# Kernel optimization log

Measured on AMD Instinct MI355X. Metric: run time of the kernel, lower is better.

## Reference

```python
import jax, jax.numpy as jnp
import numpy as np

N_DELTA, N_THETA, N_GAMMA = 2, 4, 8
N_OSC = N_DELTA + N_THETA + N_GAMMA  # 14
INPUT_DIM = 512
N_CLASSES = 2
COUPLING = 1.5
DT = 0.01
N_STEPS = 100


def _natural_freqs():
    # Natural frequencies (Hz) per EEG band: delta ~2Hz, theta ~6Hz, gamma ~40Hz
    return jnp.concatenate([
        jnp.full((N_DELTA,), 2.0, dtype=jnp.float32),
        jnp.full((N_THETA,), 6.0, dtype=jnp.float32),
        jnp.full((N_GAMMA,), 40.0, dtype=jnp.float32),
    ])


def setup_inputs() -> dict:
    key = jax.random.key(0)
    k_x, k_win, k_wc = jax.random.split(key, 3)
    x = jax.random.normal(k_x, (4096, 64, INPUT_DIM), dtype=jnp.float32)
    W_in = jax.random.normal(k_win, (INPUT_DIM, N_OSC), dtype=jnp.float32) / np.sqrt(INPUT_DIM)
    b_in = jnp.zeros((N_OSC,), dtype=jnp.float32)
    omega = _natural_freqs()
    Wc = jax.random.normal(k_wc, (N_OSC, N_CLASSES), dtype=jnp.float32) / np.sqrt(N_OSC)
    bc = jnp.zeros((N_CLASSES,), dtype=jnp.float32)
    return {"x": x, "W_in": W_in, "b_in": b_in, "omega": omega, "Wc": Wc, "bc": bc}


def reference(x, W_in, b_in, omega, Wc, bc):
    # Mean-pool over the object/token dimension: [B,S,D] -> [B,D]
    if x.ndim == 3:
        x = x.mean(axis=1)
    # Project input features to initial oscillator phases: [B,14]
    theta0 = x @ W_in + b_in
    two_pi = jnp.float32(2.0 * np.pi)
    k_over_n = jnp.float32(COUPLING / N_OSC)
    dt = jnp.float32(DT)

    def step(theta, _):
        s = jnp.sin(theta)
        c = jnp.cos(theta)
        # mean-field Kuramoto coupling: sum_j sin(th_j - th_i) = S*cos(th_i) - C*sin(th_i)
        S = s.sum(axis=-1, keepdims=True)
        C = c.sum(axis=-1, keepdims=True)
        dtheta = two_pi * omega + k_over_n * (S * c - C * s)
        return theta + dt * dtheta, None

    theta, _ = jax.lax.scan(step, theta0, None, length=N_STEPS)
    h = jnp.cos(theta)  # oscillator readout: [B,14]
    logits = h @ Wc + bc
    return jax.nn.log_softmax(logits, axis=-1)
```

## Files before the change

kernel.cpp:

```cpp
#include <hip/hip_runtime.h>
#include <math.h>

#define SEQ   64
#define DIM   512
#define NOSC  14
#define NSTEP 100

typedef float f4 __attribute__((ext_vector_type(4)));

__device__ __forceinline__ float dpp_sum16(float v) {
    v += __int_as_float(__builtin_amdgcn_update_dpp(0, __float_as_int(v), 0xB1,  0xF, 0xF, true));
    v += __int_as_float(__builtin_amdgcn_update_dpp(0, __float_as_int(v), 0x4E,  0xF, 0xF, true));
    v += __int_as_float(__builtin_amdgcn_update_dpp(0, __float_as_int(v), 0x141, 0xF, 0xF, true));
    v += __int_as_float(__builtin_amdgcn_update_dpp(0, __float_as_int(v), 0x140, 0xF, 0xF, true));
    return v;
}

__device__ __forceinline__ void fast_sincos(float theta, float* s, float* c) {
    const float inv2pi = 0.15915494309189535f;
    float r = theta * inv2pi;
    r = r - floorf(r);
    *s = __builtin_amdgcn_sinf(r);
    *c = __builtin_amdgcn_cosf(r);
}

__global__ __launch_bounds__(256)
void fused_kernel(const float* __restrict__ x,
                  const float* __restrict__ W_in,
                  const float* __restrict__ b_in,
                  const float* __restrict__ omega,
                  const float* __restrict__ Wc,
                  const float* __restrict__ bc,
                  float* __restrict__ out)
{
    const int b = blockIdx.x;
    const int t = threadIdx.x;
    const int f = t & 127;
    const int shalf = t >> 7;

    const f4* xv = reinterpret_cast<const f4*>(x + (size_t)b * (SEQ * DIM));

    f4 acc = (f4)(0.0f);
    const int s0 = shalf * 32;
#pragma unroll 8
    for (int s = s0; s < s0 + 32; ++s) {
        f4 v = __builtin_nontemporal_load(&xv[s * (DIM / 4) + f]);
        acc += v;
    }

    __shared__ float meanv[DIM];
    __shared__ f4    part[128];
    __shared__ float pp[NOSC][16];

    if (shalf == 1) part[f] = acc;
    __syncthreads();
    if (shalf == 0) {
        f4 o = part[f];
        const float inv = 1.0f / (float)SEQ;
        meanv[4 * f + 0] = (acc[0] + o[0]) * inv;
        meanv[4 * f + 1] = (acc[1] + o[1]) * inv;
        meanv[4 * f + 2] = (acc[2] + o[2]) * inv;
        meanv[4 * f + 3] = (acc[3] + o[3]) * inv;
    }
    __syncthreads();

    if (t < NOSC * 16) {
        const int o  = t >> 4;
        const int ch = t & 15;
        float p = 0.f;
#pragma unroll 8
        for (int d = ch * 32; d < ch * 32 + 32; ++d)
            p += meanv[d] * W_in[d * NOSC + o];
        pp[o][ch] = p;
    }
    __syncthreads();

    if (t >= 16) return;

    const int  o    = t;
    const bool act  = (o < NOSC);
    const float mask = act ? 1.0f : 0.0f;
    const int   oc   = act ? o : (NOSC - 1);

    float theta = 0.0f;
    if (act) {
        theta = b_in[o];
#pragma unroll
        for (int ch = 0; ch < 16; ++ch) theta += pp[o][ch];
    }

    const float drift = 6.283185307179586f * omega[oc];
    const float kn = 1.5f / (float)NOSC;
    const float dt = 0.01f;

    for (int it = 0; it < NSTEP; ++it) {
        float s_, c_;
        fast_sincos(theta, &s_, &c_);
        s_ *= mask;
        c_ *= mask;
        const float S = dpp_sum16(s_);
        const float C = dpp_sum16(c_);
        theta += dt * (drift + kn * (S * c_ - C * s_));
    }

    float hs, hc;
    fast_sincos(theta, &hs, &hc);
    const float h = hc * mask;
    float z0 = dpp_sum16(h * Wc[oc * 2 + 0]);
    float z1 = dpp_sum16(h * Wc[oc * 2 + 1]);

    if (o == 0) {
        z0 += bc[0];
        z1 += bc[1];
        const float mx  = fmaxf(z0, z1);
        const float lse = mx + logf(expf(z0 - mx) + expf(z1 - mx));
        out[(size_t)b * 2 + 0] = z0 - lse;
        out[(size_t)b * 2 + 1] = z1 - lse;
    }
}

extern "C" void kernel_launch(void* const* d_in, const int* in_sizes, int n_in,
                              void* d_out, int out_size, void* d_ws, size_t ws_size,
                              hipStream_t stream)
{
    const float* x     = (const float*)d_in[0];
    const float* W_in  = (const float*)d_in[1];
    const float* b_in  = (const float*)d_in[2];
    const float* omega = (const float*)d_in[3];
    const float* Wc    = (const float*)d_in[4];
    const float* bc    = (const float*)d_in[5];
    float* out = (float*)d_out;

    const int B = in_sizes[0] / (SEQ * DIM);

    fused_kernel<<<B, 256, 0, stream>>>(x, W_in, b_in, omega, Wc, bc, out);
}
```

Baseline: 107.2 us.

## Process two rows per block, overlapping next-row loads with ODE integration

Each block now handles two batch rows. While a wavefront (threads 192+) runs the 100-step Kuramoto integration for the current row, threads 0-127 stream and mean-pool the next row into a double-buffered shared array. The aim is to hide the serial sincos/DPP loop behind memory traffic. In exchange, each row's pooling now uses only 128 threads with 64 serial loads instead of 256, the grid is halved, and the pipeline depth is only two, so latency hiding per block is limited.

```diff
diff --git a/kernel.cpp b/kernel.cpp
--- a/kernel.cpp
+++ b/kernel.cpp
@@ -5,6 +5,7 @@
 #define DIM   512
 #define NOSC  14
 #define NSTEP 100
+#define RPB   2
 
 typedef float f4 __attribute__((ext_vector_type(4)));
 
@@ -24,98 +25,112 @@
     *c = __builtin_amdgcn_cosf(r);
 }
 
-__global__ __launch_bounds__(256)
+__global__ __launch_bounds__(256, 8)
 void fused_kernel(const float* __restrict__ x,
                   const float* __restrict__ W_in,
                   const float* __restrict__ b_in,
                   const float* __restrict__ omega,
                   const float* __restrict__ Wc,
                   const float* __restrict__ bc,
-                  float* __restrict__ out)
+                  float* __restrict__ out, int B)
 {
-    const int b = blockIdx.x;
-    const int t = threadIdx.x;
-    const int f = t & 127;
-    const int shalf = t >> 7;
+    const int t    = threadIdx.x;
+    const int row0 = blockIdx.x * RPB;
 
-    const f4* xv = reinterpret_cast<const f4*>(x + (size_t)b * (SEQ * DIM));
-
-    f4 acc = (f4)(0.0f);
-    const int s0 = shalf * 32;
-#pragma unroll 8
-    for (int s = s0; s < s0 + 32; ++s) {
-        f4 v = __builtin_nontemporal_load(&xv[s * (DIM / 4) + f]);
-        acc += v;
-    }
-
-    __shared__ float meanv[DIM];
-    __shared__ f4    part[128];
+    __shared__ f4    mv[2][DIM / 4];
     __shared__ float pp[NOSC][16];
 
-    if (shalf == 1) part[f] = acc;
+    if (t < 128 && row0 < B) {
+        const f4* xv = reinterpret_cast<const f4*>(x + (size_t)row0 * (SEQ * DIM));
+        f4 acc = (f4)(0.0f);
+#pragma unroll 4
+        for (int s = 0; s < SEQ; ++s)
+            acc += __builtin_nontemporal_load(&xv[s * (DIM / 4) + t]);
+        mv[0][t] = acc * (1.0f / SEQ);
+    }
     __syncthreads();
-    if (shalf == 0) {
-        f4 o = part[f];
-        const float inv = 1.0f / (float)SEQ;
-        meanv[4 * f + 0] = (acc[0] + o[0]) * inv;
-        meanv[4 * f + 1] = (acc[1] + o[1]) * inv;
-        meanv[4 * f + 2] = (acc[2] + o[2]) * inv;
-        meanv[4 * f + 3] = (acc[3] + o[3]) * inv;
+    {
+        const float* m = reinterpret_cast<const float*>(mv[0]);
+        if (t < NOSC * 16) {
+            const int o  = t >> 4;
+            const int ch = t & 15;
+            float p = 0.f;
+#pragma unroll 8
+            for (int i = 0; i < 32; ++i) {
+                const int d = i * 16 + ch;
+                p += m[d] * W_in[d * NOSC + o];
+            }
+            pp[o][ch] = p;
+        }
     }
     __syncthreads();
 
-    if (t < NOSC * 16) {
-        const int o  = t >> 4;
-        const int ch = t & 15;
-        float p = 0.f;
+    for (int r = 0; r < RPB; ++r) {
+        const int nb = (r & 1) ^ 1;
+        if (t >= 192) {
+            const int lane = t - 192;
+            const int row  = row0 + r;
+            if (lane < 16 && row < B) {
+                const bool  act  = (lane < NOSC);
+                const float mask = act ? 1.0f : 0.0f;
+                const int   oc   = act ? lane : (NOSC - 1);
+
+                float theta = 0.0f;
+                if (act) {
+                    theta = b_in[lane];
+#pragma unroll
+                    for (int ch = 0; ch < 16; ++ch) theta += pp[lane][ch];
+                }
+                const float drift = 6.283185307179586f * omega[oc];
+                const float kn = 1.5f / (float)NOSC;
+                const float dt = 0.01f;
+
+                for (int it = 0; it < NSTEP; ++it) {
+                    float s_, c_;
+                    fast_sincos(theta, &s_, &c_);
+                    s_ *= mask; c_ *= mask;
+                    const float S = dpp_sum16(s_);
+                    const float C = dpp_sum16(c_);
+                    theta += dt * (drift + kn * (S * c_ - C * s_));
+                }
+
+                float hs, hc;
+                fast_sincos(theta, &hs, &hc);
+                const float h = hc * mask;
+                float z0 = dpp_sum16(h * Wc[oc * 2 + 0]);
+                float z1 = dpp_sum16(h * Wc[oc * 2 + 1]);
+                if (lane == 0) {
+                    z0 += bc[0]; z1 += bc[1];
+                    const float mx  = fmaxf(z0, z1);
+                    const float lse = mx + logf(expf(z0 - mx) + expf(z1 - mx));
+                    out[(size_t)row * 2 + 0] = z0 - lse;
+                    out[(size_t)row * 2 + 1] = z1 - lse;
+                }
+            }
+        } else if (t < 128 && r + 1 < RPB && row0 + r + 1 < B) {
+            const f4* xv = reinterpret_cast<const f4*>(x + (size_t)(row0 + r + 1) * (SEQ * DIM));
+            f4 acc = (f4)(0.0f);
+#pragma unroll 4
+            for (int s = 0; s < SEQ; ++s)
+                acc += __builtin_nontemporal_load(&xv[s * (DIM / 4) + t]);
+            mv[nb][t] = acc * (1.0f / SEQ);
+        }
+        __syncthreads();
+        if (r + 1 < RPB) {
+            const float* m = reinterpret_cast<const float*>(mv[nb]);
+            if (t < NOSC * 16) {
+                const int o  = t >> 4;
+                const int ch = t & 15;
+                float p = 0.f;
 #pragma unroll 8
-        for (int d = ch * 32; d < ch * 32 + 32; ++d)
-            p += meanv[d] * W_in[d * NOSC + o];
-        pp[o][ch] = p;
-    }
-    __syncthreads();
-
-    if (t >= 16) return;
-
-    const int  o    = t;
-    const bool act  = (o < NOSC);
-    const float mask = act ? 1.0f : 0.0f;
-    const int   oc   = act ? o : (NOSC - 1);
-
-    float theta = 0.0f;
-    if (act) {
-        theta = b_in[o];
-#pragma unroll
-        for (int ch = 0; ch < 16; ++ch) theta += pp[o][ch];
-    }
-
-    const float drift = 6.283185307179586f * omega[oc];
-    const float kn = 1.5f / (float)NOSC;
-    const float dt = 0.01f;
-
-    for (int it = 0; it < NSTEP; ++it) {
-        float s_, c_;
-        fast_sincos(theta, &s_, &c_);
-        s_ *= mask;
-        c_ *= mask;
-        const float S = dpp_sum16(s_);
-        const float C = dpp_sum16(c_);
-        theta += dt * (drift + kn * (S * c_ - C * s_));
-    }
-
-    float hs, hc;
-    fast_sincos(theta, &hs, &hc);
-    const float h = hc * mask;
-    float z0 = dpp_sum16(h * Wc[oc * 2 + 0]);
-    float z1 = dpp_sum16(h * Wc[oc * 2 + 1]);
-
-    if (o == 0) {
-        z0 += bc[0];
-        z1 += bc[1];
-        const float mx  = fmaxf(z0, z1);
-        const float lse = mx + logf(expf(z0 - mx) + expf(z1 - mx));
-        out[(size_t)b * 2 + 0] = z0 - lse;
-        out[(size_t)b * 2 + 1] = z1 - lse;
+                for (int i = 0; i < 32; ++i) {
+                    const int d = i * 16 + ch;
+                    p += m[d] * W_in[d * NOSC + o];
+                }
+                pp[o][ch] = p;
+            }
+        }
+        __syncthreads();
     }
 }
 
@@ -133,5 +148,6 @@
 
     const int B = in_sizes[0] / (SEQ * DIM);
 
-    fused_kernel<<<B, 256, 0, stream>>>(x, W_in, b_in, omega, Wc, bc, out);
+    const int grid = (B + RPB - 1) / RPB;
+    fused_kernel<<<grid, 256, 0, stream>>>(x, W_in, b_in, omega, Wc, bc, out, B);
 }
```

After: 100.1 us. -6.6%, faster.
